# Performance work log

Measured on AMD Instinct MI355X. Metric: run time of the kernel, lower is better.

The kernel has to match this reference:

```python
import jax, jax.numpy as jnp
import numpy as np


def _chamfer(src, tgt):
    # src: [B, N, 3], tgt: [B, M, 3]
    x2 = jnp.sum(src * src, axis=-1)              # [B, N]
    y2 = jnp.sum(tgt * tgt, axis=-1)              # [B, M]
    xy = jnp.einsum('bnd,bmd->bnm', src, tgt)     # [B, N, M]
    d2 = x2[:, :, None] + y2[:, None, :] - 2.0 * xy
    d2 = jnp.maximum(d2, 0.0)                     # guard tiny negatives
    cham_x = jnp.min(d2, axis=2)                  # [B, N] min over tgt
    cham_y = jnp.min(d2, axis=1)                  # [B, M] min over src
    # point_reduction='mean', batch_reduction='sum'
    loss = jnp.sum(jnp.mean(cham_x, axis=1)) + jnp.sum(jnp.mean(cham_y, axis=1))
    return loss


def setup_inputs() -> dict:
    key = jax.random.key(0)
    k1, k2 = jax.random.split(key)
    src = jax.random.normal(k1, (16, 4096, 3), dtype=jnp.float32)
    tgt = jax.random.normal(k2, (16, 4096, 3), dtype=jnp.float32)
    return {"src": src, "tgt": tgt}


def reference(src, tgt):
    wgeo = 1.0
    return wgeo * _chamfer(src, tgt)
```

## Files before the change

### kernel.cpp

```cpp
#include <hip/hip_runtime.h>
#include <hip/hip_bf16.h>


#define BATCH   16
#define NPTS    4096
#define CHUNKC  1024
#define NCHUNKS (NPTS / CHUNKC)
#define NSTRIPS 16
#define NSTEP   (CHUNKC / 64)

typedef __attribute__((ext_vector_type(8)))  short short8;
typedef __attribute__((ext_vector_type(16))) float float16;

union U4S8 { uint4 u; short8 s; };

__device__ inline unsigned int bfb(float v) {
    __hip_bfloat16 h = __float2bfloat16(v);
    unsigned short u; __builtin_memcpy(&u, &h, 2);
    return (unsigned int)u;
}
__device__ inline float bff(float v) { return __bfloat162float(__float2bfloat16(v)); }

#define ONEB 0x3F80u

__device__ inline void buildA(float x, float y, float z, uint4& w0, uint4& w1) {
    float xhf = bff(x), yhf = bff(y), zhf = bff(z);
    float f = fmaf(x, x, fmaf(y, y, z * z));
    float fhf = bff(f);
    unsigned xh = bfb(xhf), yh = bfb(yhf), zh = bfb(zhf);
    unsigned xl = bfb(x - xhf), yl = bfb(y - yhf), zl = bfb(z - zhf);
    unsigned fh = bfb(fhf), fl = bfb(f - fhf);
    w0 = make_uint4(xh | (yh << 16), zh | (xh << 16),
                    yh | (zh << 16), xl | (yl << 16));
    w1 = make_uint4(zl | (fh << 16), fl | (ONEB << 16), ONEB, 0u);
}

__device__ inline void buildB(float x, float y, float z, uint4& w0, uint4& w1) {
    float xhf = bff(x), yhf = bff(y), zhf = bff(z);
    float f = fmaf(x, x, fmaf(y, y, z * z));
    float fhf = bff(f);
    unsigned a = bfb(-2.0f * xhf), b = bfb(-2.0f * yhf), c = bfb(-2.0f * zhf);
    unsigned d = bfb(-2.0f * (x - xhf)), e = bfb(-2.0f * (y - yhf)),
             g = bfb(-2.0f * (z - zhf));
    unsigned fh = bfb(fhf), fl = bfb(f - fhf);
    w0 = make_uint4(a | (b << 16), c | (d << 16),
                    e | (g << 16), a | (b << 16));
    w1 = make_uint4(c | (ONEB << 16), ONEB | (fh << 16), fl, 0u);
}

__global__ __launch_bounds__(256, 2) void chamfer_kernel(
    const float* __restrict__ src, const float* __restrict__ tgt,
    float* __restrict__ out)
{
    __shared__ uint4 sbuf[2][2][CHUNKC];
    __shared__ float wsum[4];

    int blk = blockIdx.x;
    const int strip = blk & (NSTRIPS - 1); blk >>= 4;
    const int b     = blk & 15;            blk >>= 4;
    const int dir   = blk;

    const int t    = threadIdx.x;
    const int lane = t & 63;
    const int w    = t >> 6;
    const int half = lane >> 5;
    const int l5   = lane & 31;

    const float* Araw = (dir ? tgt : src) + (size_t)b * NPTS * 3;
    const float* Braw = (dir ? src : tgt) + (size_t)b * NPTS * 3;

    short8 afr[2];
#pragma unroll
    for (int g = 0; g < 2; g++) {
        int row = strip * 256 + g * 128 + w * 32 + l5;
        uint4 w0, w1;
        buildA(Araw[3 * row], Araw[3 * row + 1], Araw[3 * row + 2], w0, w1);
        U4S8 tt; tt.u = half ? w1 : w0;
        afr[g] = tt.s;
    }

    float nx[4][3];
    auto loadRaw = [&](int c) {
#pragma unroll
        for (int k = 0; k < 4; k++) {
            int p = c * CHUNKC + t + k * 256;
            nx[k][0] = Braw[3 * p + 0];
            nx[k][1] = Braw[3 * p + 1];
            nx[k][2] = Braw[3 * p + 2];
        }
    };
    auto convertWrite = [&](int bi) {
#pragma unroll
        for (int k = 0; k < 4; k++) {
            int lp = t + k * 256;
            uint4 w0, w1;
            buildB(nx[k][0], nx[k][1], nx[k][2], w0, w1);
            sbuf[bi][0][lp] = w0;
            sbuf[bi][1][lp] = w1;
        }
    };

    const float16 z16 = {0.f,0.f,0.f,0.f,0.f,0.f,0.f,0.f,
                         0.f,0.f,0.f,0.f,0.f,0.f,0.f,0.f};
    float rm[2][16];
#pragma unroll
    for (int g = 0; g < 2; g++)
#pragma unroll
        for (int r = 0; r < 16; r++) rm[g][r] = 1e30f;

    loadRaw(0);
    convertWrite(0);
    for (int c = 0; c < NCHUNKS; c++) {
        __syncthreads();
        if (c + 1 < NCHUNKS) loadRaw(c + 1);
        const int bi = c & 1;

        U4S8 c0, c1, n0, n1;
        c0.u = sbuf[bi][half][l5];
        c1.u = sbuf[bi][half][32 + l5];
#pragma unroll 4
        for (int j2 = 0; j2 < NSTEP; j2++) {
            int nj = (j2 + 1) & (NSTEP - 1);
            n0.u = sbuf[bi][half][nj * 64 + l5];
            n1.u = sbuf[bi][half][nj * 64 + 32 + l5];
            float16 a00 = __builtin_amdgcn_mfma_f32_32x32x16_bf16(afr[0], c0.s, z16, 0, 0, 0);
            float16 a01 = __builtin_amdgcn_mfma_f32_32x32x16_bf16(afr[0], c1.s, z16, 0, 0, 0);
            float16 a10 = __builtin_amdgcn_mfma_f32_32x32x16_bf16(afr[1], c0.s, z16, 0, 0, 0);
            float16 a11 = __builtin_amdgcn_mfma_f32_32x32x16_bf16(afr[1], c1.s, z16, 0, 0, 0);
#pragma unroll
            for (int r = 0; r < 16; r++) {
                rm[0][r] = fminf(fminf(a00[r], a01[r]), rm[0][r]);
                rm[1][r] = fminf(fminf(a10[r], a11[r]), rm[1][r]);
            }
            c0 = n0; c1 = n1;
        }
        if (c + 1 < NCHUNKS) convertWrite((c + 1) & 1);
    }

#pragma unroll
    for (int mask = 1; mask <= 16; mask <<= 1)
#pragma unroll
        for (int g = 0; g < 2; g++)
#pragma unroll
            for (int r = 0; r < 16; r++)
                rm[g][r] = fminf(rm[g][r], __shfl_xor(rm[g][r], mask, 64));

    float s = 0.0f;
#pragma unroll
    for (int g = 0; g < 2; g++)
#pragma unroll
        for (int r = 0; r < 16; r++) s += fmaxf(rm[g][r], 0.0f);
    s += __shfl_xor(s, 32, 64);

    if (lane == 0) wsum[w] = s;
    __syncthreads();
    if (t == 0)
        atomicAdd(out, (wsum[0] + wsum[1] + wsum[2] + wsum[3]) * (1.0f / (float)NPTS));
}

extern "C" void kernel_launch(void* const* d_in, const int* in_sizes, int n_in,
                              void* d_out, int out_size, void* d_ws, size_t ws_size,
                              hipStream_t stream)
{
    const float* src = (const float*)d_in[0];
    const float* tgt = (const float*)d_in[1];
    float* out = (float*)d_out;

    hipMemsetAsync(out, 0, sizeof(float), stream);
    chamfer_kernel<<<2 * BATCH * NSTRIPS, 256, 0, stream>>>(src, tgt, out);
}
```

Measured before the change: 79.19 us.

## Compute both chamfer directions from one distance pass using column atomicMin

Result: slower. 82.50 us (+4.2%).

```diff
diff --git a/kernel.cpp b/kernel.cpp
--- a/kernel.cpp
+++ b/kernel.cpp
@@ -4,9 +4,9 @@
 
 #define BATCH   16
 #define NPTS    4096
-#define CHUNKC  1024
+#define NSTRIPS 32
+#define CHUNKC  512
 #define NCHUNKS (NPTS / CHUNKC)
-#define NSTRIPS 16
 #define NSTEP   (CHUNKC / 64)
 
 typedef __attribute__((ext_vector_type(8)))  short short8;
@@ -48,41 +48,54 @@
     w1 = make_uint4(c | (ONEB << 16), ONEB | (fh << 16), fl, 0u);
 }
 
-__global__ __launch_bounds__(256, 2) void chamfer_kernel(
+__device__ inline float tree16(const float16& a) {
+    float m0 = fminf(fminf(a[0],  a[1]),  a[2]);
+    float m1 = fminf(fminf(a[3],  a[4]),  a[5]);
+    float m2 = fminf(fminf(a[6],  a[7]),  a[8]);
+    float m3 = fminf(fminf(a[9],  a[10]), a[11]);
+    float m4 = fminf(fminf(a[12], a[13]), a[14]);
+    float p0 = fminf(fminf(m0, m1), a[15]);
+    float p1 = fminf(fminf(m2, m3), m4);
+    return fminf(p0, p1);
+}
+
+__global__ __launch_bounds__(256, 3) void chamfer_main(
     const float* __restrict__ src, const float* __restrict__ tgt,
-    float* __restrict__ out)
+    unsigned* __restrict__ wsC, float* __restrict__ out)
 {
     __shared__ uint4 sbuf[2][2][CHUNKC];
+    __shared__ unsigned colpart[NPTS];
     __shared__ float wsum[4];
 
     int blk = blockIdx.x;
-    const int strip = blk & (NSTRIPS - 1); blk >>= 4;
-    const int b     = blk & 15;            blk >>= 4;
-    const int dir   = blk;
+    const int strip = blk & (NSTRIPS - 1);
+    const int b     = blk >> 5;
 
     const int t    = threadIdx.x;
     const int lane = t & 63;
     const int w    = t >> 6;
-    const int half = lane >> 5;
+    const int h    = lane >> 5;
     const int l5   = lane & 31;
 
-    const float* Araw = (dir ? tgt : src) + (size_t)b * NPTS * 3;
-    const float* Braw = (dir ? src : tgt) + (size_t)b * NPTS * 3;
-
-    short8 afr[2];
-#pragma unroll
-    for (int g = 0; g < 2; g++) {
-        int row = strip * 256 + g * 128 + w * 32 + l5;
+    const float* Araw = src + (size_t)b * NPTS * 3;
+    const float* Braw = tgt + (size_t)b * NPTS * 3;
+
+    short8 afr;
+    {
+        int row = strip * 128 + w * 32 + l5;
         uint4 w0, w1;
         buildA(Araw[3 * row], Araw[3 * row + 1], Araw[3 * row + 2], w0, w1);
-        U4S8 tt; tt.u = half ? w1 : w0;
-        afr[g] = tt.s;
+        U4S8 tt; tt.u = h ? w1 : w0;
+        afr = tt.s;
     }
 
-    float nx[4][3];
+#pragma unroll
+    for (int i = 0; i < 16; i++) colpart[t + i * 256] = 0xFFFFFFFFu;
+
+    float nx[2][3];
     auto loadRaw = [&](int c) {
 #pragma unroll
-        for (int k = 0; k < 4; k++) {
+        for (int k = 0; k < 2; k++) {
             int p = c * CHUNKC + t + k * 256;
             nx[k][0] = Braw[3 * p + 0];
             nx[k][1] = Braw[3 * p + 1];
@@ -91,7 +104,7 @@
     };
     auto convertWrite = [&](int bi) {
 #pragma unroll
-        for (int k = 0; k < 4; k++) {
+        for (int k = 0; k < 2; k++) {
             int lp = t + k * 256;
             uint4 w0, w1;
             buildB(nx[k][0], nx[k][1], nx[k][2], w0, w1);
@@ -102,11 +115,9 @@
 
     const float16 z16 = {0.f,0.f,0.f,0.f,0.f,0.f,0.f,0.f,
                          0.f,0.f,0.f,0.f,0.f,0.f,0.f,0.f};
-    float rm[2][16];
-#pragma unroll
-    for (int g = 0; g < 2; g++)
-#pragma unroll
-        for (int r = 0; r < 16; r++) rm[g][r] = 1e30f;
+    float rm[16];
+#pragma unroll
+    for (int r = 0; r < 16; r++) rm[r] = 1e30f;
 
     loadRaw(0);
     convertWrite(0);
@@ -116,45 +127,66 @@
         const int bi = c & 1;
 
         U4S8 c0, c1, n0, n1;
-        c0.u = sbuf[bi][half][l5];
-        c1.u = sbuf[bi][half][32 + l5];
+        c0.u = sbuf[bi][h][l5];
+        c1.u = sbuf[bi][h][32 + l5];
 #pragma unroll 4
         for (int j2 = 0; j2 < NSTEP; j2++) {
             int nj = (j2 + 1) & (NSTEP - 1);
-            n0.u = sbuf[bi][half][nj * 64 + l5];
-            n1.u = sbuf[bi][half][nj * 64 + 32 + l5];
-            float16 a00 = __builtin_amdgcn_mfma_f32_32x32x16_bf16(afr[0], c0.s, z16, 0, 0, 0);
-            float16 a01 = __builtin_amdgcn_mfma_f32_32x32x16_bf16(afr[0], c1.s, z16, 0, 0, 0);
-            float16 a10 = __builtin_amdgcn_mfma_f32_32x32x16_bf16(afr[1], c0.s, z16, 0, 0, 0);
-            float16 a11 = __builtin_amdgcn_mfma_f32_32x32x16_bf16(afr[1], c1.s, z16, 0, 0, 0);
-#pragma unroll
-            for (int r = 0; r < 16; r++) {
-                rm[0][r] = fminf(fminf(a00[r], a01[r]), rm[0][r]);
-                rm[1][r] = fminf(fminf(a10[r], a11[r]), rm[1][r]);
-            }
+            n0.u = sbuf[bi][h][nj * 64 + l5];
+            n1.u = sbuf[bi][h][nj * 64 + 32 + l5];
+            float16 a0 = __builtin_amdgcn_mfma_f32_32x32x16_bf16(afr, c0.s, z16, 0, 0, 0);
+            float16 a1 = __builtin_amdgcn_mfma_f32_32x32x16_bf16(afr, c1.s, z16, 0, 0, 0);
+#pragma unroll
+            for (int r = 0; r < 16; r++)
+                rm[r] = fminf(fminf(a0[r], a1[r]), rm[r]);
+            float cm0 = tree16(a0);
+            float cm1 = tree16(a1);
+            const int col = c * CHUNKC + j2 * 64 + l5;
+            atomicMin(&colpart[col],      __float_as_uint(fmaxf(cm0, 0.0f)));
+            atomicMin(&colpart[col + 32], __float_as_uint(fmaxf(cm1, 0.0f)));
             c0 = n0; c1 = n1;
         }
         if (c + 1 < NCHUNKS) convertWrite((c + 1) & 1);
     }
 
+    __syncthreads();
+#pragma unroll
+    for (int i = 0; i < 16; i++) {
+        const int idx = t + i * 256;
+        atomicMin(&wsC[(size_t)b * NPTS + idx], colpart[idx]);
+    }
+
 #pragma unroll
     for (int mask = 1; mask <= 16; mask <<= 1)
 #pragma unroll
-        for (int g = 0; g < 2; g++)
-#pragma unroll
-            for (int r = 0; r < 16; r++)
-                rm[g][r] = fminf(rm[g][r], __shfl_xor(rm[g][r], mask, 64));
+        for (int r = 0; r < 16; r++)
+            rm[r] = fminf(rm[r], __shfl_xor(rm[r], mask, 64));
 
     float s = 0.0f;
 #pragma unroll
-    for (int g = 0; g < 2; g++)
-#pragma unroll
-        for (int r = 0; r < 16; r++) s += fmaxf(rm[g][r], 0.0f);
+    for (int r = 0; r < 16; r++) s += fmaxf(rm[r], 0.0f);
     s += __shfl_xor(s, 32, 64);
 
     if (lane == 0) wsum[w] = s;
     __syncthreads();
     if (t == 0)
+        atomicAdd(out, (wsum[0] + wsum[1] + wsum[2] + wsum[3]) * (1.0f / (float)NPTS));
+}
+
+__global__ __launch_bounds__(256) void finish_reduce(
+    const unsigned* __restrict__ wsC, float* __restrict__ out)
+{
+    __shared__ float wsum[4];
+    const int b = blockIdx.x;
+    float v = 0.0f;
+#pragma unroll
+    for (int i = 0; i < 16; i++)
+        v += __uint_as_float(wsC[(size_t)b * NPTS + threadIdx.x + i * 256]);
+#pragma unroll
+    for (int mask = 1; mask <= 32; mask <<= 1) v += __shfl_xor(v, mask, 64);
+    if ((threadIdx.x & 63) == 0) wsum[threadIdx.x >> 6] = v;
+    __syncthreads();
+    if (threadIdx.x == 0)
         atomicAdd(out, (wsum[0] + wsum[1] + wsum[2] + wsum[3]) * (1.0f / (float)NPTS));
 }
 
@@ -165,7 +197,10 @@
     const float* src = (const float*)d_in[0];
     const float* tgt = (const float*)d_in[1];
     float* out = (float*)d_out;
+    unsigned* wsC = (unsigned*)d_ws;
 
     hipMemsetAsync(out, 0, sizeof(float), stream);
-    chamfer_kernel<<<2 * BATCH * NSTRIPS, 256, 0, stream>>>(src, tgt, out);
-}
+    hipMemsetAsync(wsC, 0xFF, (size_t)BATCH * NPTS * sizeof(unsigned), stream);
+    chamfer_main <<<BATCH * NSTRIPS, 256, 0, stream>>>(src, tgt, wsC, out);
+    finish_reduce<<<BATCH, 256, 0, stream>>>(wsC, out);
+}
```
